# Kernel optimization log

Measured on AMD Instinct MI355X. Metric: run time of the kernel, lower is better.

Reference implementation:

```python
import jax, jax.numpy as jnp
import numpy as np

HIDDEN = 64


def setup_inputs() -> dict:
    key = jax.random.key(0)
    ks = jax.random.split(key, 6)
    N, F, E = 1500, 64, 65536
    embed = jax.random.normal(ks[0], (N, F), dtype=jnp.float32)
    edge_index = jax.random.randint(ks[1], (2, E), 0, N, dtype=jnp.int64)
    # uniform noise in (0,1) for the concrete (Gumbel-sigmoid) sample
    noise = jax.random.uniform(ks[2], (N * N,), dtype=jnp.float32,
                               minval=1e-6, maxval=1.0 - 1e-6)
    tmp = jnp.float32(1.0)  # temperature beta
    # explainer MLP params: Linear(2F, 64) + ReLU, Linear(64, 1)
    W1 = jax.random.normal(ks[3], (2 * F, HIDDEN), dtype=jnp.float32) * 0.1
    b1 = jnp.zeros((HIDDEN,), dtype=jnp.float32)
    W2 = jax.random.normal(ks[4], (HIDDEN, 1), dtype=jnp.float32) * 0.1
    b2 = jnp.zeros((1,), dtype=jnp.float32)
    return {"embed": embed, "edge_index": edge_index, "noise": noise,
            "tmp": tmp, "W1": W1, "b1": b1, "W2": W2, "b2": b2}


def reference(embed, edge_index, noise, tmp, W1, b1, W2, b2):
    N, F = embed.shape
    # concat([f1, f2]) @ W1 == f1 @ W1[:F] + f2 @ W1[F:]  (same math,
    # avoids materializing the [N*N, 2F] concat explicitly)
    h1 = embed @ W1[:F]          # [N, 64] contribution of row node i
    h2 = embed @ W1[F:]          # [N, 64] contribution of col node j
    h = jax.nn.relu(h1[:, None, :] + h2[None, :, :] + b1)   # [N, N, 64]
    log_alpha = jnp.einsum('ijk,k->ij', h, W2[:, 0]) + b2[0]  # [N, N]
    log_alpha = log_alpha.reshape(-1)
    # concrete sample (training=True): sigmoid((log eps - log(1-eps) + omega)/beta)
    gate = jax.nn.sigmoid((jnp.log(noise) - jnp.log1p(-noise) + log_alpha) / tmp)
    mask = gate.reshape(N, N)
    sym_mask = (mask + mask.T) * 0.5
    edge_mask = sym_mask[edge_index[0], edge_index[1]]       # [E]
    return edge_mask
```

## Files before the change

kernel.cpp:

```cpp
#include <hip/hip_runtime.h>
#include <cmath>

#define N_NODES 1500

__global__ void pg_compute_h(const float* __restrict__ embed,
                             const float* __restrict__ W1,
                             const float* __restrict__ b1,
                             float* __restrict__ h1pb,
                             float* __restrict__ h2t) {
    const int i = blockIdx.x;
    const int t = threadIdx.x;
    const int k = t & 63;
    const int half = t >> 6;

    __shared__ float emb_s[64];
    if (t < 64) emb_s[t] = embed[i * 64 + t];
    __syncthreads();

    const float* wcol = W1 + (half << 6) * 64 + k;
    float a0 = (half == 0) ? b1[k] : 0.0f;
    float a1 = 0.0f, a2 = 0.0f, a3 = 0.0f;
#pragma unroll
    for (int f = 0; f < 64; f += 4) {
        a0 = fmaf(emb_s[f + 0], wcol[(f + 0) * 64], a0);
        a1 = fmaf(emb_s[f + 1], wcol[(f + 1) * 64], a1);
        a2 = fmaf(emb_s[f + 2], wcol[(f + 2) * 64], a2);
        a3 = fmaf(emb_s[f + 3], wcol[(f + 3) * 64], a3);
    }
    const float acc = (a0 + a1) + (a2 + a3);
    if (half == 0) h1pb[i * 64 + k] = acc;
    else           h2t[i * 64 + k]  = acc;
}

__global__ void pg_edge4(const int* __restrict__ e0,
                         const int* __restrict__ e1,
                         const float* __restrict__ noise,
                         const float* __restrict__ tmp_p,
                         const float* __restrict__ W2,
                         const float* __restrict__ b2,
                         const float4* __restrict__ h1pb4,
                         const float4* __restrict__ h2t4,
                         float* __restrict__ out,
                         int E) {
    const int tid  = blockIdx.x * blockDim.x + threadIdx.x;
    const int wave = tid >> 6;
    const int lane = threadIdx.x & 63;
    const int q    = lane >> 4;
    const int l    = lane & 15;

    const int e     = wave * 4 + q;
    const bool valid = (e < E);
    const int ee    = valid ? e : 0;

    const int r = e0[ee];
    const int c = e1[ee];

    float nrc = 0.5f, ncr = 0.5f;
    if (l == 0) {
        nrc = noise[r * N_NODES + c];
        ncr = noise[c * N_NODES + r];
    }

    const float4 w2v = ((const float4*)W2)[l];

    const float4 fa = h1pb4[r * 16 + l];
    const float4 fb = h2t4[c * 16 + l];
    const float4 ra = h1pb4[c * 16 + l];
    const float4 rb = h2t4[r * 16 + l];

    float p = fmaxf(fa.x + fb.x, 0.0f) * w2v.x;
    p = fmaf(fmaxf(fa.y + fb.y, 0.0f), w2v.y, p);
    p = fmaf(fmaxf(fa.z + fb.z, 0.0f), w2v.z, p);
    p = fmaf(fmaxf(fa.w + fb.w, 0.0f), w2v.w, p);

    float s = fmaxf(ra.x + rb.x, 0.0f) * w2v.x;
    s = fmaf(fmaxf(ra.y + rb.y, 0.0f), w2v.y, s);
    s = fmaf(fmaxf(ra.z + rb.z, 0.0f), w2v.z, s);
    s = fmaf(fmaxf(ra.w + rb.w, 0.0f), w2v.w, s);

#pragma unroll
    for (int off = 1; off <= 8; off <<= 1) {
        p += __shfl_xor(p, off, 64);
        s += __shfl_xor(s, off, 64);
    }

    if (valid && l == 0) {
        const float bb    = b2[0];
        const float inv_t = 1.0f / tmp_p[0];
        const float la1 = p + bb;
        const float la2 = s + bb;
        const float x1 = (__logf(nrc / (1.0f - nrc)) + la1) * inv_t;
        const float x2 = (__logf(ncr / (1.0f - ncr)) + la2) * inv_t;
        const float g1 = 1.0f / (1.0f + __expf(-x1));
        const float g2 = 1.0f / (1.0f + __expf(-x2));
        out[e] = 0.5f * (g1 + g2);
    }
}

extern "C" void kernel_launch(void* const* d_in, const int* in_sizes, int n_in,
                              void* d_out, int out_size, void* d_ws, size_t ws_size,
                              hipStream_t stream) {
    const float* embed = (const float*)d_in[0];
    const int*   eidx  = (const int*)d_in[1];
    const float* noise = (const float*)d_in[2];
    const float* tmp_p = (const float*)d_in[3];
    const float* W1    = (const float*)d_in[4];
    const float* b1    = (const float*)d_in[5];
    const float* W2    = (const float*)d_in[6];
    const float* b2    = (const float*)d_in[7];
    float* out = (float*)d_out;

    const int E = in_sizes[1] / 2;
    const int* e0 = eidx;
    const int* e1 = eidx + E;

    float* h1pb = (float*)d_ws;
    float* h2t  = h1pb + N_NODES * 64;

    pg_compute_h<<<N_NODES, 128, 0, stream>>>(embed, W1, b1, h1pb, h2t);

    const int edges_per_block = 16;
    const int grid = (E + edges_per_block - 1) / edges_per_block;
    pg_edge4<<<grid, 256, 0, stream>>>(e0, e1, noise, tmp_p, W2, b2,
                                       (const float4*)h1pb, (const float4*)h2t,
                                       out, E);
}
```

Before: 16.28 us.

## Store hidden tables as interleaved bf16 and process eight edges per wave

The per-node h1 and h2 tables are now written as bfloat16 and interleaved into one 128-element row per node, halving their footprint and letting each edge gather its row and column data as contiguous 16-byte loads. The edge kernel now assigns 8 lanes per edge instead of 16, so a wave handles 8 edges, and the block covers 32 edges. Its reduction is restructured so that the forward and reverse logits are summed in the same shuffle chain, with two lanes computing the two gates. This lowers gather traffic and shuffle work per edge, at the cost of bf16 rounding of intermediate activations, which may shift results slightly.

```diff
diff --git a/kernel.cpp b/kernel.cpp
--- a/kernel.cpp
+++ b/kernel.cpp
@@ -1,4 +1,5 @@
 #include <hip/hip_runtime.h>
+#include <hip/hip_bf16.h>
 #include <cmath>
 
 #define N_NODES 1500
@@ -6,8 +7,7 @@
 __global__ void pg_compute_h(const float* __restrict__ embed,
                              const float* __restrict__ W1,
                              const float* __restrict__ b1,
-                             float* __restrict__ h1pb,
-                             float* __restrict__ h2t) {
+                             __hip_bfloat16* __restrict__ htab) {
     const int i = blockIdx.x;
     const int t = threadIdx.x;
     const int k = t & 63;
@@ -28,73 +28,86 @@
         a3 = fmaf(emb_s[f + 3], wcol[(f + 3) * 64], a3);
     }
     const float acc = (a0 + a1) + (a2 + a3);
-    if (half == 0) h1pb[i * 64 + k] = acc;
-    else           h2t[i * 64 + k]  = acc;
+    htab[i * 128 + half * 64 + k] = __float2bfloat16(acc);
 }
 
-__global__ void pg_edge4(const int* __restrict__ e0,
+__device__ __forceinline__ float blo(unsigned u) {
+    union { unsigned i; float f; } v; v.i = u << 16; return v.f;
+}
+__device__ __forceinline__ float bhi(unsigned u) {
+    union { unsigned i; float f; } v; v.i = u & 0xffff0000u; return v.f;
+}
+
+__global__ void pg_edge8(const int* __restrict__ e0,
                          const int* __restrict__ e1,
                          const float* __restrict__ noise,
                          const float* __restrict__ tmp_p,
                          const float* __restrict__ W2,
                          const float* __restrict__ b2,
-                         const float4* __restrict__ h1pb4,
-                         const float4* __restrict__ h2t4,
+                         const ushort* __restrict__ htab,
                          float* __restrict__ out,
                          int E) {
     const int tid  = blockIdx.x * blockDim.x + threadIdx.x;
     const int wave = tid >> 6;
     const int lane = threadIdx.x & 63;
-    const int q    = lane >> 4;
-    const int l    = lane & 15;
+    const int g    = lane >> 3;
+    const int l    = lane & 7;
 
-    const int e     = wave * 4 + q;
+    const int e     = wave * 8 + g;
     const bool valid = (e < E);
     const int ee    = valid ? e : 0;
 
     const int r = e0[ee];
     const int c = e1[ee];
 
-    float nrc = 0.5f, ncr = 0.5f;
-    if (l == 0) {
-        nrc = noise[r * N_NODES + c];
-        ncr = noise[c * N_NODES + r];
+    const float bb    = b2[0];
+    const float inv_t = 1.0f / tmp_p[0];
+
+    float nv = 0.5f;
+    if (l < 2) nv = noise[(l == 0) ? (r * N_NODES + c) : (c * N_NODES + r)];
+
+    const uint4* hr = (const uint4*)(htab + r * 128);
+    const uint4* hc = (const uint4*)(htab + c * 128);
+    const uint4 h1r = hr[l];
+    const uint4 h2r = hr[l + 8];
+    const uint4 h1c = hc[l];
+    const uint4 h2c = hc[l + 8];
+
+    const float4 w2a = ((const float4*)W2)[l * 2];
+    const float4 w2b = ((const float4*)W2)[l * 2 + 1];
+
+    float p = fmaxf(blo(h1r.x) + blo(h2c.x), 0.0f) * w2a.x;
+    p = fmaf(fmaxf(bhi(h1r.x) + bhi(h2c.x), 0.0f), w2a.y, p);
+    p = fmaf(fmaxf(blo(h1r.y) + blo(h2c.y), 0.0f), w2a.z, p);
+    p = fmaf(fmaxf(bhi(h1r.y) + bhi(h2c.y), 0.0f), w2a.w, p);
+    p = fmaf(fmaxf(blo(h1r.z) + blo(h2c.z), 0.0f), w2b.x, p);
+    p = fmaf(fmaxf(bhi(h1r.z) + bhi(h2c.z), 0.0f), w2b.y, p);
+    p = fmaf(fmaxf(blo(h1r.w) + blo(h2c.w), 0.0f), w2b.z, p);
+    p = fmaf(fmaxf(bhi(h1r.w) + bhi(h2c.w), 0.0f), w2b.w, p);
+
+    float s = fmaxf(blo(h1c.x) + blo(h2r.x), 0.0f) * w2a.x;
+    s = fmaf(fmaxf(bhi(h1c.x) + bhi(h2r.x), 0.0f), w2a.y, s);
+    s = fmaf(fmaxf(blo(h1c.y) + blo(h2r.y), 0.0f), w2a.z, s);
+    s = fmaf(fmaxf(bhi(h1c.y) + bhi(h2r.y), 0.0f), w2a.w, s);
+    s = fmaf(fmaxf(blo(h1c.z) + blo(h2r.z), 0.0f), w2b.x, s);
+    s = fmaf(fmaxf(bhi(h1c.z) + bhi(h2r.z), 0.0f), w2b.y, s);
+    s = fmaf(fmaxf(blo(h1c.w) + blo(h2r.w), 0.0f), w2b.z, s);
+    s = fmaf(fmaxf(bhi(h1c.w) + bhi(h2r.w), 0.0f), w2b.w, s);
+
+    const bool odd = (l & 1);
+    float w = odd ? s : p;
+    float z = odd ? p : s;
+    w += __shfl_xor(z, 1, 64);
+    w += __shfl_xor(w, 2, 64);
+    w += __shfl_xor(w, 4, 64);
+
+    float gate = 0.0f;
+    if (l < 2) {
+        const float x = (__logf(nv / (1.0f - nv)) + w + bb) * inv_t;
+        gate = 1.0f / (1.0f + __expf(-x));
     }
-
-    const float4 w2v = ((const float4*)W2)[l];
-
-    const float4 fa = h1pb4[r * 16 + l];
-    const float4 fb = h2t4[c * 16 + l];
-    const float4 ra = h1pb4[c * 16 + l];
-    const float4 rb = h2t4[r * 16 + l];
-
-    float p = fmaxf(fa.x + fb.x, 0.0f) * w2v.x;
-    p = fmaf(fmaxf(fa.y + fb.y, 0.0f), w2v.y, p);
-    p = fmaf(fmaxf(fa.z + fb.z, 0.0f), w2v.z, p);
-    p = fmaf(fmaxf(fa.w + fb.w, 0.0f), w2v.w, p);
-
-    float s = fmaxf(ra.x + rb.x, 0.0f) * w2v.x;
-    s = fmaf(fmaxf(ra.y + rb.y, 0.0f), w2v.y, s);
-    s = fmaf(fmaxf(ra.z + rb.z, 0.0f), w2v.z, s);
-    s = fmaf(fmaxf(ra.w + rb.w, 0.0f), w2v.w, s);
-
-#pragma unroll
-    for (int off = 1; off <= 8; off <<= 1) {
-        p += __shfl_xor(p, off, 64);
-        s += __shfl_xor(s, off, 64);
-    }
-
-    if (valid && l == 0) {
-        const float bb    = b2[0];
-        const float inv_t = 1.0f / tmp_p[0];
-        const float la1 = p + bb;
-        const float la2 = s + bb;
-        const float x1 = (__logf(nrc / (1.0f - nrc)) + la1) * inv_t;
-        const float x2 = (__logf(ncr / (1.0f - ncr)) + la2) * inv_t;
-        const float g1 = 1.0f / (1.0f + __expf(-x1));
-        const float g2 = 1.0f / (1.0f + __expf(-x2));
-        out[e] = 0.5f * (g1 + g2);
-    }
+    const float gother = __shfl_xor(gate, 1, 64);
+    if (valid && l == 0) out[e] = 0.5f * (gate + gother);
 }
 
 extern "C" void kernel_launch(void* const* d_in, const int* in_sizes, int n_in,
@@ -114,14 +127,12 @@
     const int* e0 = eidx;
     const int* e1 = eidx + E;
 
-    float* h1pb = (float*)d_ws;
-    float* h2t  = h1pb + N_NODES * 64;
+    __hip_bfloat16* htab = (__hip_bfloat16*)d_ws;
 
-    pg_compute_h<<<N_NODES, 128, 0, stream>>>(embed, W1, b1, h1pb, h2t);
+    pg_compute_h<<<N_NODES, 128, 0, stream>>>(embed, W1, b1, htab);
 
-    const int edges_per_block = 16;
+    const int edges_per_block = 32;
     const int grid = (E + edges_per_block - 1) / edges_per_block;
-    pg_edge4<<<grid, 256, 0, stream>>>(e0, e1, noise, tmp_p, W2, b2,
-                                       (const float4*)h1pb, (const float4*)h2t,
-                                       out, E);
+    pg_edge8<<<grid, 256, 0, stream>>>(e0, e1, noise, tmp_p, W2, b2,
+                                       (const ushort*)htab, out, E);
 }
```

Result: faster. 14.10 us (-13.4%).
